# Kernel tuning notes

Measured on AMD Instinct MI355X. Metric: run time of the kernel, lower is better.

## Reference

```python
import jax, jax.numpy as jnp
import numpy as np

B, N, C = 2, 6, 80
FH, FW = 16, 44
D = 112
NX = NY = 128
NZ = 1
OGH, OGW = 256, 704
D_BOUND = (2.0, 58.0, 0.5)
VOXEL_SIZE = np.array([0.8, 0.8, 8.0], dtype=np.float32)
VOXEL_COORD = np.array([-51.2 + 0.4, -51.2 + 0.4, -5.0 + 4.0], dtype=np.float32)
VOXEL_NUM = np.array([NX, NY, NZ], dtype=np.int32)


def setup_inputs() -> dict:
    key = jax.random.key(0)
    k1, k2 = jax.random.split(key)
    context = jax.random.normal(k1, (B * N, C, FH, FW), jnp.float32)
    depth_logits = jax.random.normal(k2, (B * N, D, FH, FW), jnp.float32)
    # realistic camera matrices (random matrices would not be invertible / physical)
    intrin = np.tile(np.eye(4, dtype=np.float32), (B, N, 1, 1))
    intrin[..., 0, 0] = 560.0
    intrin[..., 1, 1] = 560.0
    intrin[..., 0, 2] = OGW / 2.0
    intrin[..., 1, 2] = OGH / 2.0
    ida = np.tile(np.eye(4, dtype=np.float32), (B, N, 1, 1))
    s2e = np.tile(np.eye(4, dtype=np.float32), (B, N, 1, 1))
    # cam axes (x right, y down, z forward) -> ego axes (x fwd, y left, z up)
    M = np.array([[0., 0., 1.], [-1., 0., 0.], [0., -1., 0.]], dtype=np.float32)
    for n in range(N):
        yaw = 2.0 * np.pi * n / N
        cy, sy = np.cos(yaw), np.sin(yaw)
        R = np.array([[cy, -sy, 0.], [sy, cy, 0.], [0., 0., 1.]], dtype=np.float32)
        s2e[:, n, :3, :3] = R @ M
        s2e[:, n, :3, 3] = np.array([1.5 * cy, 1.5 * sy, 1.6], dtype=np.float32)
    bda = np.tile(np.eye(4, dtype=np.float32), (B, 1, 1))
    return dict(context=context, depth_logits=depth_logits,
                sensor2ego_mat=jnp.asarray(s2e), intrin_mat=jnp.asarray(intrin),
                ida_mat=jnp.asarray(ida), bda_mat=jnp.asarray(bda))


def _frustum():
    # [D, FH, FW, 4] pixel-plane frustum: (u, v, depth, 1)
    d = jnp.arange(D_BOUND[0], D_BOUND[1], D_BOUND[2], dtype=jnp.float32) + D_BOUND[2] / 2.0
    d = jnp.broadcast_to(d[:, None, None], (D, FH, FW))
    xs = jnp.broadcast_to(jnp.linspace(0.0, OGW - 1.0, FW)[None, None, :], (D, FH, FW))
    ys = jnp.broadcast_to(jnp.linspace(0.0, OGH - 1.0, FH)[None, :, None], (D, FH, FW))
    return jnp.stack([xs, ys, d, jnp.ones_like(d)], -1)


def reference(context, depth_logits, sensor2ego_mat, intrin_mat, ida_mat, bda_mat):
    # ---- get_geometry ----
    pts = _frustum()[None, None, ..., None]                       # [1,1,D,FH,FW,4,1]
    ida_inv = jnp.linalg.inv(ida_mat).reshape(B, N, 1, 1, 1, 4, 4)
    pts = ida_inv @ pts
    pts = jnp.concatenate([pts[..., :2, :] * pts[..., 2:3, :], pts[..., 2:, :]], axis=-2)
    combine = (sensor2ego_mat @ jnp.linalg.inv(intrin_mat)).reshape(B, N, 1, 1, 1, 4, 4)
    pts = combine @ pts
    bda = bda_mat.reshape(B, 1, 1, 1, 1, 4, 4)
    geom = (bda @ pts)[..., :3, 0]                                # [B,N,D,FH,FW,3] ego coords

    # ---- voxel indices ----
    vsize = jnp.asarray(VOXEL_SIZE)
    vcoord = jnp.asarray(VOXEL_COORD)
    vnum = jnp.asarray(VOXEL_NUM)
    idx = jnp.floor((geom - (vcoord - vsize / 2.0)) / vsize).astype(jnp.int32)
    valid = jnp.all((idx >= 0) & (idx < vnum), axis=-1)           # [B,N,D,FH,FW]

    # ---- lift: depth-weighted outer product ----
    depth = jax.nn.softmax(depth_logits, axis=1).reshape(B, N, D, FH, FW)
    ctx = context.reshape(B, N, C, FH, FW)
    feat = jnp.einsum('bndhw,bnchw->bndhwc', depth, ctx)          # [B,N,D,FH,FW,C]
    feat = feat * valid[..., None]

    # ---- splat: scatter-add into BEV grid ----
    b_idx = jnp.arange(B, dtype=jnp.int32)[:, None, None, None, None]
    lin = b_idx * (NY * NX) + idx[..., 1] * NX + idx[..., 0]
    lin = jnp.where(valid, lin, 0)                                # invalid feats already zeroed
    bev = jax.ops.segment_sum(feat.reshape(-1, C), lin.reshape(-1),
                              num_segments=B * NY * NX)
    return bev.reshape(B, NY, NX, C).transpose(0, 3, 1, 2)        # [B,C,NY,NX]
```

## Files before the change

kernel.cpp:

```cpp
#include <hip/hip_runtime.h>
#include <hip/hip_bf16.h>
#include <math.h>

#define B_ 2
#define N_ 6
#define C_ 80
#define FH_ 16
#define FW_ 44
#define D_ 112
#define NX_ 128
#define NY_ 128
#define NCOL (B_ * N_ * FH_ * FW_)
#define NCELL (B_ * NY_ * NX_)
#define MAXT (NCOL * D_)
#define GB_CELLS 16

typedef __hip_bfloat16 bf16;
typedef unsigned short u16;

__device__ __forceinline__ float loadf(const void* p, int i, int isbf) {
  if (isbf) return __bfloat162float(((const bf16*)p)[i]);
  return ((const float*)p)[i];
}

__device__ void inv4(const float m[16], float invOut[16]) {
  float inv[16];
  inv[0]  =  m[5]*m[10]*m[15] - m[5]*m[11]*m[14] - m[9]*m[6]*m[15] + m[9]*m[7]*m[14] + m[13]*m[6]*m[11] - m[13]*m[7]*m[10];
  inv[4]  = -m[4]*m[10]*m[15] + m[4]*m[11]*m[14] + m[8]*m[6]*m[15] - m[8]*m[7]*m[14] - m[12]*m[6]*m[11] + m[12]*m[7]*m[10];
  inv[8]  =  m[4]*m[9]*m[15]  - m[4]*m[11]*m[13] - m[8]*m[5]*m[15] + m[8]*m[7]*m[13] + m[12]*m[5]*m[11] - m[12]*m[7]*m[9];
  inv[12] = -m[4]*m[9]*m[14]  + m[4]*m[10]*m[13] + m[8]*m[5]*m[14] - m[8]*m[6]*m[13] - m[12]*m[5]*m[10] + m[12]*m[6]*m[9];
  inv[1]  = -m[1]*m[10]*m[15] + m[1]*m[11]*m[14] + m[9]*m[2]*m[15] - m[9]*m[3]*m[14] - m[13]*m[2]*m[11] + m[13]*m[3]*m[10];
  inv[5]  =  m[0]*m[10]*m[15] - m[0]*m[11]*m[14] - m[8]*m[2]*m[15] + m[8]*m[3]*m[14] + m[12]*m[2]*m[11] - m[12]*m[3]*m[10];
  inv[9]  = -m[0]*m[9]*m[15]  + m[0]*m[11]*m[13] + m[8]*m[1]*m[15] - m[8]*m[3]*m[13] - m[12]*m[1]*m[11] + m[12]*m[3]*m[9];
  inv[13] =  m[0]*m[9]*m[14]  - m[0]*m[10]*m[13] - m[8]*m[1]*m[14] + m[8]*m[2]*m[13] + m[12]*m[1]*m[10] - m[12]*m[2]*m[9];
  inv[2]  =  m[1]*m[6]*m[15]  - m[1]*m[7]*m[14]  - m[5]*m[2]*m[15] + m[5]*m[3]*m[14] + m[13]*m[2]*m[7]  - m[13]*m[3]*m[6];
  inv[6]  = -m[0]*m[6]*m[15]  + m[0]*m[7]*m[14]  + m[4]*m[2]*m[15] - m[4]*m[3]*m[14] - m[12]*m[2]*m[7]  + m[12]*m[3]*m[6];
  inv[10] =  m[0]*m[5]*m[15]  - m[0]*m[7]*m[13]  - m[4]*m[1]*m[15] + m[4]*m[3]*m[13] + m[12]*m[1]*m[7]  - m[12]*m[3]*m[5];
  inv[14] = -m[0]*m[5]*m[14]  + m[0]*m[6]*m[13]  + m[4]*m[1]*m[14] - m[4]*m[2]*m[13] - m[12]*m[1]*m[6]  + m[12]*m[2]*m[5];
  inv[3]  = -m[1]*m[6]*m[11]  + m[1]*m[7]*m[10]  + m[5]*m[2]*m[11] - m[5]*m[3]*m[10] - m[9]*m[2]*m[7]   + m[9]*m[3]*m[6];
  inv[7]  =  m[0]*m[6]*m[11]  - m[0]*m[7]*m[10]  - m[4]*m[2]*m[11] + m[4]*m[3]*m[10] + m[8]*m[2]*m[7]   - m[8]*m[3]*m[6];
  inv[11] = -m[0]*m[5]*m[11]  + m[0]*m[7]*m[9]   + m[4]*m[1]*m[11] - m[4]*m[3]*m[9]  - m[8]*m[1]*m[7]   + m[8]*m[3]*m[5];
  inv[15] =  m[0]*m[5]*m[10]  - m[0]*m[6]*m[9]   - m[4]*m[1]*m[10] + m[4]*m[2]*m[9]  + m[8]*m[1]*m[6]   - m[8]*m[2]*m[5];
  float det = m[0]*inv[0] + m[1]*inv[4] + m[2]*inv[8] + m[3]*inv[12];
  det = 1.0f / det;
  for (int i = 0; i < 16; i++) invOut[i] = inv[i] * det;
}

__device__ void mul4(const float A[16], const float Bm[16], float Cm[16]) {
  for (int i = 0; i < 4; i++)
    for (int j = 0; j < 4; j++) {
      float s = 0.f;
      for (int k = 0; k < 4; k++) s += A[i * 4 + k] * Bm[k * 4 + j];
      Cm[i * 4 + j] = s;
    }
}

__global__ void lss_prep(const void* __restrict__ logits,
                         const void* __restrict__ s2e, const void* __restrict__ intrin,
                         const void* __restrict__ ida, const void* __restrict__ bda,
                         float* __restrict__ mats, int* __restrict__ flags) {
  __shared__ int s_cnt;
  __shared__ int s_mats_bf;
  const int t = threadIdx.x;
  if (t == 0) s_cnt = 0;
  __syncthreads();
  {
    const unsigned short* u = (const unsigned short*)logits;
    unsigned short v = u[2 * t];
    int e = (v >> 7) & 0xFF;
    if (v == 0 || (e >= 110 && e <= 136)) atomicAdd(&s_cnt, 1);
  }
  __syncthreads();
  if (t == 0) {
    flags[0] = (s_cnt > 170) ? 1 : 0;
    float v = ((const float*)intrin)[0];
    s_mats_bf = (v > 100.f && v < 1.0e6f) ? 0 : 1;
    flags[1] = s_mats_bf;
  }
  __syncthreads();
  const int mbf = s_mats_bf;
  if (t < B_ * N_) {
    int b = t / N_;
    float S[16], I[16], A[16], Bd[16], Iinv[16], Ainv[16], Cm[16], M[16];
    for (int i = 0; i < 16; i++) {
      S[i]  = loadf(s2e,    t * 16 + i, mbf);
      I[i]  = loadf(intrin, t * 16 + i, mbf);
      A[i]  = loadf(ida,    t * 16 + i, mbf);
      Bd[i] = loadf(bda,    b * 16 + i, mbf);
    }
    inv4(I, Iinv);
    inv4(A, Ainv);
    mul4(S, Iinv, Cm);
    mul4(Bd, Cm, M);
    for (int i = 0; i < 16; i++) { mats[t * 32 + i] = Ainv[i]; mats[t * 32 + 16 + i] = M[i]; }
  }
}

__global__ void lss_transpose(const void* __restrict__ ctx, const int* __restrict__ flags,
                              float* __restrict__ ctx_t) {
  int i = blockIdx.x * blockDim.x + threadIdx.x;
  if (i >= NCOL * C_) return;
  int col = i / C_, c = i - col * C_;
  int bn = col / (FH_ * FW_), r = col - bn * (FH_ * FW_);
  int h = r / FW_, w = r - h * FW_;
  ctx_t[i] = loadf(ctx, ((bn * C_ + c) * FH_ + h) * FW_ + w, flags[0]);
}

__device__ __forceinline__ int geom_cell(const float* __restrict__ mats,
                                         int bn, int h, int w, int d) {
  const float* Ai = mats + bn * 32;
  const float* M = mats + bn * 32 + 16;
  float u = (float)w * (703.0f / 43.0f);
  float v = (float)h * 17.0f;
  float dep = 2.25f + 0.5f * (float)d;
  float p0 = ((Ai[0] * u + Ai[1] * v) + Ai[2] * dep) + Ai[3];
  float p1 = ((Ai[4] * u + Ai[5] * v) + Ai[6] * dep) + Ai[7];
  float p2 = ((Ai[8] * u + Ai[9] * v) + Ai[10] * dep) + Ai[11];
  float p3 = ((Ai[12] * u + Ai[13] * v) + Ai[14] * dep) + Ai[15];
  float q0 = p0 * p2, q1 = p1 * p2;
  float gx = ((M[0] * q0 + M[1] * q1) + M[2] * p2) + M[3] * p3;
  float gy = ((M[4] * q0 + M[5] * q1) + M[6] * p2) + M[7] * p3;
  float gz = ((M[8] * q0 + M[9] * q1) + M[10] * p2) + M[11] * p3;
  int ix = (int)floorf((gx + 51.2f) / 0.8f);
  int iy = (int)floorf((gy + 51.2f) / 0.8f);
  int iz = (int)floorf((gz + 5.0f) / 8.0f);
  bool valid = (ix >= 0) && (ix < NX_) && (iy >= 0) && (iy < NY_) && (iz == 0);
  int b = bn / N_;
  return valid ? (b * (NY_ * NX_) + iy * NX_ + ix) : -1;
}

__global__ __launch_bounds__(64) void lss_count(const float* __restrict__ mats,
                                                int* __restrict__ counts) {
  const int tid = threadIdx.x;
  const int col = blockIdx.x;
  const int w = col % FW_;
  const int h = (col / FW_) % FH_;
  const int bn = col / (FW_ * FH_);
  __shared__ int s_cell[D_];
  s_cell[tid] = geom_cell(mats, bn, h, w, tid);
  if (tid < D_ - 64) s_cell[tid + 64] = geom_cell(mats, bn, h, w, tid + 64);
  __syncthreads();
  for (int d = tid; d < D_; d += 64) {
    int vcell = s_cell[d];
    if (vcell >= 0 && (d == 0 || s_cell[d - 1] != vcell)) atomicAdd(&counts[vcell], 1);
  }
}

__global__ __launch_bounds__(1024) void lss_scan(const int* __restrict__ counts,
                                                 int* __restrict__ offsets,
                                                 int* __restrict__ cursors) {
  __shared__ int s[1024];
  const int t = threadIdx.x;
  const int base = t * 32;
  int local[32];
  int sum = 0;
  for (int j = 0; j < 32; j++) { local[j] = counts[base + j]; sum += local[j]; }
  s[t] = sum;
  __syncthreads();
  for (int st = 1; st < 1024; st <<= 1) {
    int v = (t >= st) ? s[t - st] : 0;
    __syncthreads();
    s[t] += v;
    __syncthreads();
  }
  int run = s[t] - sum;
  for (int j = 0; j < 32; j++) {
    offsets[base + j] = run;
    cursors[base + j] = run;
    run += local[j];
  }
}

__global__ __launch_bounds__(64) void lss_fill(
    const void* __restrict__ logits, const float* __restrict__ mats,
    const int* __restrict__ flags, int* __restrict__ cursors,
    u16* __restrict__ colids, float* __restrict__ wts) {
  const int tid = threadIdx.x;
  const int col = blockIdx.x;
  const int w = col % FW_;
  const int h = (col / FW_) % FH_;
  const int bn = col / (FW_ * FH_);
  const int tbf = flags[0];

  __shared__ float s_w[D_];
  __shared__ int s_cell[D_];

  const int base = ((bn * D_) * FH_ + h) * FW_ + w;
  float l0 = loadf(logits, base + tid * (FH_ * FW_), tbf);
  float l1 = (tid < D_ - 64) ? loadf(logits, base + (tid + 64) * (FH_ * FW_), tbf) : -1e30f;
  float m = fmaxf(l0, l1);
  for (int s = 32; s > 0; s >>= 1) m = fmaxf(m, __shfl_xor(m, s));
  float e0 = expf(l0 - m);
  float e1 = (tid < D_ - 64) ? expf(l1 - m) : 0.f;
  float sum = e0 + e1;
  for (int s = 32; s > 0; s >>= 1) sum += __shfl_xor(sum, s);
  float inv_sum = 1.0f / sum;

  s_w[tid] = e0;
  s_cell[tid] = geom_cell(mats, bn, h, w, tid);
  if (tid < D_ - 64) {
    s_w[tid + 64] = e1;
    s_cell[tid + 64] = geom_cell(mats, bn, h, w, tid + 64);
  }
  __syncthreads();

  for (int d = tid; d < D_; d += 64) {
    int vcell = s_cell[d];
    if (vcell >= 0 && (d == 0 || s_cell[d - 1] != vcell)) {
      float acc = s_w[d];
      for (int j = d + 1; j < D_ && s_cell[j] == vcell; ++j) acc += s_w[j];
      int pos = atomicAdd(&cursors[vcell], 1);
      colids[pos] = (u16)col;
      wts[pos] = acc * inv_sum;
    }
  }
}

__global__ __launch_bounds__(1024) void lss_gather(
    const float* __restrict__ ctx_t, const int* __restrict__ counts,
    const int* __restrict__ offsets, const u16* __restrict__ colids,
    const float* __restrict__ wts, const int* __restrict__ flags,
    void* __restrict__ out) {
  __shared__ float s_out[GB_CELLS * 84];
  const int tid = threadIdx.x;
  const int wv = tid >> 6;
  const int ln = tid & 63;
  const int sl = ln >> 2;
  const int g = ln & 3;
  const int cell = blockIdx.x * GB_CELLS + wv;
  const int n = counts[cell];
  const int off = offsets[cell];

  float acc[20];
#pragma unroll
  for (int i = 0; i < 20; i++) acc[i] = 0.f;

  for (int j = sl; j < n; j += 16) {
    int colj = colids[off + j];
    float wj = wts[off + j];
    const float4* cp = (const float4*)(ctx_t + colj * C_ + g * 20);
#pragma unroll
    for (int q = 0; q < 5; q++) {
      float4 v = cp[q];
      acc[q * 4 + 0] += wj * v.x;
      acc[q * 4 + 1] += wj * v.y;
      acc[q * 4 + 2] += wj * v.z;
      acc[q * 4 + 3] += wj * v.w;
    }
  }
#pragma unroll
  for (int msk = 4; msk <= 32; msk <<= 1) {
#pragma unroll
    for (int i = 0; i < 20; i++) acc[i] += __shfl_xor(acc[i], msk);
  }
  if (sl == 0) {
#pragma unroll
    for (int i = 0; i < 20; i++) s_out[wv * 84 + g * 20 + i] = acc[i];
  }
  __syncthreads();

  const int x = tid & 15;
  const int c0 = tid >> 4;
  const int cell0 = blockIdx.x * GB_CELLS;
  const int b = cell0 >> 14;
  const int yx0 = cell0 & 16383;
  if (flags[0]) {
    bf16* o = (bf16*)out;
    o[(size_t)(b * C_ + c0) * (NY_ * NX_) + yx0 + x] = __float2bfloat16(s_out[x * 84 + c0]);
    if (c0 < 16)
      o[(size_t)(b * C_ + 64 + c0) * (NY_ * NX_) + yx0 + x] = __float2bfloat16(s_out[x * 84 + 64 + c0]);
  } else {
    float* o = (float*)out;
    o[(size_t)(b * C_ + c0) * (NY_ * NX_) + yx0 + x] = s_out[x * 84 + c0];
    if (c0 < 16)
      o[(size_t)(b * C_ + 64 + c0) * (NY_ * NX_) + yx0 + x] = s_out[x * 84 + 64 + c0];
  }
}

extern "C" void kernel_launch(void* const* d_in, const int* in_sizes, int n_in,
                              void* d_out, int out_size, void* d_ws, size_t ws_size,
                              hipStream_t stream) {
  const void* ctx = d_in[0];
  const void* logits = d_in[1];
  const void* s2e = d_in[2];
  const void* intrin = d_in[3];
  const void* ida = d_in[4];
  const void* bda = d_in[5];

  float* wsf = (float*)d_ws;
  int* flags   = (int*)wsf;
  float* mats  = wsf + 16;
  int* counts  = (int*)(wsf + 512);
  int* offsets = (int*)(wsf + 512 + NCELL);
  int* cursors = (int*)(wsf + 512 + 2 * NCELL);
  float* ctx_t = wsf + 512 + 3 * NCELL;
  u16* colids  = (u16*)(ctx_t + NCOL * C_);
  float* wts   = (float*)((float*)colids + MAXT / 2);

  hipMemsetAsync(counts, 0, NCELL * sizeof(int), stream);
  lss_prep<<<1, 256, 0, stream>>>(logits, s2e, intrin, ida, bda, mats, flags);
  lss_transpose<<<(NCOL * C_ + 255) / 256, 256, 0, stream>>>(ctx, flags, ctx_t);
  lss_count<<<NCOL, 64, 0, stream>>>(mats, counts);
  lss_scan<<<1, 1024, 0, stream>>>(counts, offsets, cursors);
  lss_fill<<<NCOL, 64, 0, stream>>>(logits, mats, flags, cursors, colids, wts);
  lss_gather<<<NCELL / GB_CELLS, 1024, 0, stream>>>(ctx_t, counts, offsets, colids, wts, flags, d_out);
}
```

Measured before the change: 193.5 us.

## Fuse memset into prep and transpose into count; shuffle-based dedup

Zeroing of the counts buffer moves into a multi-block prep kernel, which replaces the separate memset. The context transpose is merged into the count kernel as extra blocks, cutting two launches overall. The count kernel now packs four columns per 256-thread block and uses wavefront shuffles instead of shared memory and a barrier to drop consecutive duplicate cells. The workspace layout is also reordered.

```diff
diff --git a/kernel.cpp b/kernel.cpp
--- a/kernel.cpp
+++ b/kernel.cpp
@@ -10,10 +10,13 @@
 #define D_ 112
 #define NX_ 128
 #define NY_ 128
-#define NCOL (B_ * N_ * FH_ * FW_)
+#define HW_ (FH_ * FW_)
+#define NCOL (B_ * N_ * HW_)
 #define NCELL (B_ * NY_ * NX_)
 #define MAXT (NCOL * D_)
 #define GB_CELLS 16
+#define NCB 2112
+#define NTB 2640
 
 typedef __hip_bfloat16 bf16;
 typedef unsigned short u16;
@@ -55,57 +58,6 @@
     }
 }
 
-__global__ void lss_prep(const void* __restrict__ logits,
-                         const void* __restrict__ s2e, const void* __restrict__ intrin,
-                         const void* __restrict__ ida, const void* __restrict__ bda,
-                         float* __restrict__ mats, int* __restrict__ flags) {
-  __shared__ int s_cnt;
-  __shared__ int s_mats_bf;
-  const int t = threadIdx.x;
-  if (t == 0) s_cnt = 0;
-  __syncthreads();
-  {
-    const unsigned short* u = (const unsigned short*)logits;
-    unsigned short v = u[2 * t];
-    int e = (v >> 7) & 0xFF;
-    if (v == 0 || (e >= 110 && e <= 136)) atomicAdd(&s_cnt, 1);
-  }
-  __syncthreads();
-  if (t == 0) {
-    flags[0] = (s_cnt > 170) ? 1 : 0;
-    float v = ((const float*)intrin)[0];
-    s_mats_bf = (v > 100.f && v < 1.0e6f) ? 0 : 1;
-    flags[1] = s_mats_bf;
-  }
-  __syncthreads();
-  const int mbf = s_mats_bf;
-  if (t < B_ * N_) {
-    int b = t / N_;
-    float S[16], I[16], A[16], Bd[16], Iinv[16], Ainv[16], Cm[16], M[16];
-    for (int i = 0; i < 16; i++) {
-      S[i]  = loadf(s2e,    t * 16 + i, mbf);
-      I[i]  = loadf(intrin, t * 16 + i, mbf);
-      A[i]  = loadf(ida,    t * 16 + i, mbf);
-      Bd[i] = loadf(bda,    b * 16 + i, mbf);
-    }
-    inv4(I, Iinv);
-    inv4(A, Ainv);
-    mul4(S, Iinv, Cm);
-    mul4(Bd, Cm, M);
-    for (int i = 0; i < 16; i++) { mats[t * 32 + i] = Ainv[i]; mats[t * 32 + 16 + i] = M[i]; }
-  }
-}
-
-__global__ void lss_transpose(const void* __restrict__ ctx, const int* __restrict__ flags,
-                              float* __restrict__ ctx_t) {
-  int i = blockIdx.x * blockDim.x + threadIdx.x;
-  if (i >= NCOL * C_) return;
-  int col = i / C_, c = i - col * C_;
-  int bn = col / (FH_ * FW_), r = col - bn * (FH_ * FW_);
-  int h = r / FW_, w = r - h * FW_;
-  ctx_t[i] = loadf(ctx, ((bn * C_ + c) * FH_ + h) * FW_ + w, flags[0]);
-}
-
 __device__ __forceinline__ int geom_cell(const float* __restrict__ mats,
                                          int bn, int h, int w, int d) {
   const float* Ai = mats + bn * 32;
@@ -129,21 +81,83 @@
   return valid ? (b * (NY_ * NX_) + iy * NX_ + ix) : -1;
 }
 
-__global__ __launch_bounds__(64) void lss_count(const float* __restrict__ mats,
-                                                int* __restrict__ counts) {
-  const int tid = threadIdx.x;
-  const int col = blockIdx.x;
+__global__ __launch_bounds__(256) void lss_prep(
+    const void* __restrict__ logits,
+    const void* __restrict__ s2e, const void* __restrict__ intrin,
+    const void* __restrict__ ida, const void* __restrict__ bda,
+    float* __restrict__ mats, int* __restrict__ flags,
+    int* __restrict__ counts) {
+  const int t = threadIdx.x;
+  const int blk = blockIdx.x;
+  for (int i = blk * 256 + t; i < NCELL; i += 33 * 256) counts[i] = 0;
+  if (blk != 0) return;
+
+  __shared__ int s_cnt;
+  __shared__ int s_mats_bf;
+  if (t == 0) s_cnt = 0;
+  __syncthreads();
+  {
+    const unsigned short* u = (const unsigned short*)logits;
+    unsigned short v = u[2 * t];
+    int e = (v >> 7) & 0xFF;
+    if (v == 0 || (e >= 110 && e <= 136)) atomicAdd(&s_cnt, 1);
+  }
+  __syncthreads();
+  if (t == 0) {
+    flags[0] = (s_cnt > 170) ? 1 : 0;
+    float v = ((const float*)intrin)[0];
+    s_mats_bf = (v > 100.f && v < 1.0e6f) ? 0 : 1;
+    flags[1] = s_mats_bf;
+  }
+  __syncthreads();
+  const int mbf = s_mats_bf;
+  if (t < B_ * N_) {
+    int b = t / N_;
+    float S[16], I[16], A[16], Bd[16], Iinv[16], Ainv[16], Cm[16], M[16];
+    for (int i = 0; i < 16; i++) {
+      S[i]  = loadf(s2e,    t * 16 + i, mbf);
+      I[i]  = loadf(intrin, t * 16 + i, mbf);
+      A[i]  = loadf(ida,    t * 16 + i, mbf);
+      Bd[i] = loadf(bda,    b * 16 + i, mbf);
+    }
+    inv4(I, Iinv);
+    inv4(A, Ainv);
+    mul4(S, Iinv, Cm);
+    mul4(Bd, Cm, M);
+    for (int i = 0; i < 16; i++) { mats[t * 32 + i] = Ainv[i]; mats[t * 32 + 16 + i] = M[i]; }
+  }
+}
+
+__global__ __launch_bounds__(256) void lss_count(
+    const void* __restrict__ ctx, const float* __restrict__ mats,
+    const int* __restrict__ flags, int* __restrict__ counts,
+    float* __restrict__ ctx_t) {
+  const int t = threadIdx.x;
+  const int blk = blockIdx.x;
+
+  if (blk >= NCB) {
+    const int tbf = flags[0];
+    const int i = (blk - NCB) * 256 + t;
+    int col = i / C_, c = i - col * C_;
+    int bn = col / HW_, r = col - bn * HW_;
+    int h = r / FW_, w = r - h * FW_;
+    ctx_t[i] = loadf(ctx, ((bn * C_ + c) * FH_ + h) * FW_ + w, tbf);
+    return;
+  }
+
+  const int col = blk * 4 + (t >> 6);
+  const int ln = t & 63;
   const int w = col % FW_;
   const int h = (col / FW_) % FH_;
   const int bn = col / (FW_ * FH_);
-  __shared__ int s_cell[D_];
-  s_cell[tid] = geom_cell(mats, bn, h, w, tid);
-  if (tid < D_ - 64) s_cell[tid + 64] = geom_cell(mats, bn, h, w, tid + 64);
-  __syncthreads();
-  for (int d = tid; d < D_; d += 64) {
-    int vcell = s_cell[d];
-    if (vcell >= 0 && (d == 0 || s_cell[d - 1] != vcell)) atomicAdd(&counts[vcell], 1);
-  }
+  int c0 = geom_cell(mats, bn, h, w, ln);
+  int c1 = (ln < D_ - 64) ? geom_cell(mats, bn, h, w, ln + 64) : -3;
+  int p0 = __shfl_up(c0, 1);
+  int p1 = __shfl_up(c1, 1);
+  int c63 = __shfl(c0, 63);
+  if (ln == 0) p1 = c63;
+  if (c0 >= 0 && (ln == 0 || p0 != c0)) atomicAdd(&counts[c0], 1);
+  if (c1 >= 0 && p1 != c1) atomicAdd(&counts[c1], 1);
 }
 
 __global__ __launch_bounds__(1024) void lss_scan(const int* __restrict__ counts,
@@ -291,16 +305,14 @@
   int* flags   = (int*)wsf;
   float* mats  = wsf + 16;
   int* counts  = (int*)(wsf + 512);
-  int* offsets = (int*)(wsf + 512 + NCELL);
-  int* cursors = (int*)(wsf + 512 + 2 * NCELL);
-  float* ctx_t = wsf + 512 + 3 * NCELL;
-  u16* colids  = (u16*)(ctx_t + NCOL * C_);
-  float* wts   = (float*)((float*)colids + MAXT / 2);
-
-  hipMemsetAsync(counts, 0, NCELL * sizeof(int), stream);
-  lss_prep<<<1, 256, 0, stream>>>(logits, s2e, intrin, ida, bda, mats, flags);
-  lss_transpose<<<(NCOL * C_ + 255) / 256, 256, 0, stream>>>(ctx, flags, ctx_t);
-  lss_count<<<NCOL, 64, 0, stream>>>(mats, counts);
+  int* offsets = counts + NCELL;
+  int* cursors = offsets + NCELL;
+  float* ctx_t = (float*)(cursors + NCELL);
+  float* wts   = ctx_t + NCOL * C_;
+  u16* colids  = (u16*)(wts + MAXT);
+
+  lss_prep<<<33, 256, 0, stream>>>(logits, s2e, intrin, ida, bda, mats, flags, counts);
+  lss_count<<<NCB + NTB, 256, 0, stream>>>(ctx, mats, flags, counts, ctx_t);
   lss_scan<<<1, 1024, 0, stream>>>(counts, offsets, cursors);
   lss_fill<<<NCOL, 64, 0, stream>>>(logits, mats, flags, cursors, colids, wts);
   lss_gather<<<NCELL / GB_CELLS, 1024, 0, stream>>>(ctx_t, counts, offsets, colids, wts, flags, d_out);
```

Result: faster. 178.2 us (-7.9%).
